# Optimization experiments

Measured on AMD Instinct MI355X. Metric: run time of the kernel, lower is better.

The kernel has to match this reference:

```python
import jax, jax.numpy as jnp
import numpy as np

H = 512      # hidden_size
NH = 8       # head_size (num heads)
DH = H // NH # att_size per head
FFN = 2048
B, S = 8, 1024
NEG = -1e9
EPS = 1e-5


def _layernorm(x, g, b):
    mu = jnp.mean(x, axis=-1, keepdims=True)
    var = jnp.var(x, axis=-1, keepdims=True)
    return (x - mu) * jax.lax.rsqrt(var + EPS) * g + b


def setup_inputs() -> dict:
    key = jax.random.key(0)
    ks = jax.random.split(key, 16)
    s = 0.02
    return {
        "x": jax.random.normal(ks[0], (B, S, H), jnp.float32),
        "attn_bias": jax.random.normal(ks[1], (B, S, S), jnp.float32),
        "graph_mask": jax.random.randint(ks[2], (B, S, S), 0, 2, jnp.int32),
        "ln1_g": jnp.ones((H,), jnp.float32),
        "ln1_b": jnp.zeros((H,), jnp.float32),
        "Wq": jax.random.normal(ks[3], (H, H), jnp.float32) * s,
        "bq": jnp.zeros((H,), jnp.float32),
        "Wk": jax.random.normal(ks[4], (H, H), jnp.float32) * s,
        "bk": jnp.zeros((H,), jnp.float32),
        "Wv": jax.random.normal(ks[5], (H, H), jnp.float32) * s,
        "bv": jnp.zeros((H,), jnp.float32),
        "Wo": jax.random.normal(ks[6], (H, H), jnp.float32) * s,
        "bo": jnp.zeros((H,), jnp.float32),
        "ln2_g": jnp.ones((H,), jnp.float32),
        "ln2_b": jnp.zeros((H,), jnp.float32),
        "W1": jax.random.normal(ks[7], (H, FFN), jnp.float32) * s,
        "b1": jnp.zeros((FFN,), jnp.float32),
        "W2": jax.random.normal(ks[8], (FFN, H), jnp.float32) * s,
        "b2": jnp.zeros((H,), jnp.float32),
    }


def reference(x, attn_bias, graph_mask, ln1_g, ln1_b, Wq, bq, Wk, bk, Wv, bv,
              Wo, bo, ln2_g, ln2_b, W1, b1, W2, b2):
    b, s, h = x.shape
    # --- self-attention block (eval mode: dropouts are identity) ---
    y = _layernorm(x, ln1_g, ln1_b)
    q = (y @ Wq + bq).reshape(b, s, NH, DH).transpose(0, 2, 1, 3)  # [B,h,S,d]
    k = (y @ Wk + bk).reshape(b, s, NH, DH).transpose(0, 2, 1, 3)
    v = (y @ Wv + bv).reshape(b, s, NH, DH).transpose(0, 2, 1, 3)
    scale = DH ** -0.5
    scores = jnp.einsum('bhqd,bhkd->bhqk', q * scale, k)  # [B,h,S,S]
    mask = (graph_mask == 0)[:, None, :, :]               # [B,1,S,S] broadcast over heads
    bias = jnp.where(mask, NEG, attn_bias[:, None, :, :])
    scores = scores + bias
    scores = jnp.where(mask, NEG, scores)
    p = jax.nn.softmax(scores, axis=-1)
    o = jnp.einsum('bhqk,bhkd->bhqd', p, v)
    o = o.transpose(0, 2, 1, 3).reshape(b, s, h) @ Wo + bo
    x = x + o
    # --- FFN block ---
    y = _layernorm(x, ln2_g, ln2_b)
    y = jax.nn.gelu(y @ W1 + b1, approximate=False) @ W2 + b2
    return x + y
```

## Files before the change

### kernel.cpp

```cpp
#include <hip/hip_runtime.h>
#include <hip/hip_bf16.h>
#include <type_traits>

static constexpr int kS   = 1024;
static constexpr int kH   = 512;
static constexpr int kFFN = 2048;

using bf16 = __hip_bfloat16;
using short8  = __attribute__((ext_vector_type(8))) short;
using float4v = __attribute__((ext_vector_type(4))) float;
#define MFMA16 __builtin_amdgcn_mfma_f32_16x16x32_bf16

__device__ __forceinline__ unsigned short f2bfu(float f){
  unsigned int u = __float_as_uint(f);
  return (unsigned short)((u + 0x7fffu + ((u >> 16) & 1u)) >> 16);
}
__device__ __forceinline__ float bfu2f(unsigned short u){
  return __uint_as_float(((unsigned int)u) << 16);
}
__device__ __forceinline__ unsigned int pack2(float a, float b){
  return (unsigned int)f2bfu(a) | ((unsigned int)f2bfu(b) << 16);
}
__device__ __forceinline__ void async16(const void* g, void* l){
  __builtin_amdgcn_global_load_lds(
    (const __attribute__((address_space(1))) unsigned int*)g,
    (__attribute__((address_space(3))) unsigned int*)l, 16, 0, 0);
}
__device__ __forceinline__ int swz(int col, int row){
  return (col & ~63) | (((((col>>3)&7) ^ (row&7)))<<3) | (col&7);
}

__device__ __forceinline__ void ln_row(const float* __restrict__ x,
    const float* __restrict__ g, const float* __restrict__ bb,
    bf16* __restrict__ y, long row, int lane){
  const float* xr = x + row * kH + lane*8;
  float4 a = *(const float4*)xr, c = *(const float4*)(xr+4);
  float v[8] = {a.x,a.y,a.z,a.w,c.x,c.y,c.z,c.w};
  float s=0.f, s2=0.f;
#pragma unroll
  for(int i=0;i<8;i++){ s += v[i]; s2 += v[i]*v[i]; }
#pragma unroll
  for(int o=32; o>=1; o>>=1){ s += __shfl_xor(s,o,64); s2 += __shfl_xor(s2,o,64); }
  float mu  = s * (1.f/kH);
  float rs  = rsqrtf(s2*(1.f/kH) - mu*mu + 1e-5f);
  float gv[8], bv[8];
  {
    float4 t0=*(const float4*)(g+lane*8),  t1=*(const float4*)(g+lane*8+4);
    float4 t2=*(const float4*)(bb+lane*8), t3=*(const float4*)(bb+lane*8+4);
    gv[0]=t0.x;gv[1]=t0.y;gv[2]=t0.z;gv[3]=t0.w;gv[4]=t1.x;gv[5]=t1.y;gv[6]=t1.z;gv[7]=t1.w;
    bv[0]=t2.x;bv[1]=t2.y;bv[2]=t2.z;bv[3]=t2.w;bv[4]=t3.x;bv[5]=t3.y;bv[6]=t3.z;bv[7]=t3.w;
  }
  unsigned int ow[4];
#pragma unroll
  for(int i=0;i<4;i++){
    float a0 = (v[2*i]  -mu)*rs*gv[2*i]   + bv[2*i];
    float a1 = (v[2*i+1]-mu)*rs*gv[2*i+1] + bv[2*i+1];
    ow[i] = pack2(a0, a1);
  }
  *reinterpret_cast<uint4*>(y + row*kH + swz(lane*8, (int)row)) = make_uint4(ow[0],ow[1],ow[2],ow[3]);
}

__global__ __launch_bounds__(256) void ln_kernel(const float* __restrict__ x,
    const float* __restrict__ g, const float* __restrict__ bb, bf16* __restrict__ y){
  ln_row(x, g, bb, y, (long)blockIdx.x*4 + (threadIdx.x>>6), threadIdx.x&63);
}

__device__ __forceinline__ void prep_tile(const float* __restrict__ W,
    bf16* __restrict__ WT, int K, int N, int kb, int nb){
  __shared__ unsigned short Ts[64*68];
  int tid=threadIdx.x;
  {
    int k=tid>>2, nc=(tid&3)*16;
    const float* p = W + (size_t)(kb+k)*N + nb+nc;
#pragma unroll
    for(int i=0;i<16;i+=4){
      float4 f = *(const float4*)(p+i);
      Ts[k*68+nc+i  ]=f2bfu(f.x); Ts[k*68+nc+i+1]=f2bfu(f.y);
      Ts[k*68+nc+i+2]=f2bfu(f.z); Ts[k*68+nc+i+3]=f2bfu(f.w);
    }
  }
  __syncthreads();
  {
    int n=tid>>2, kc=(tid&3)*16;
    unsigned short tmp[16];
#pragma unroll
    for(int i=0;i<16;i++) tmp[i] = Ts[(kc+i)*68 + n];
    int row = nb+n, kg0 = kc>>3;
    bf16* op = WT + (size_t)row*K + kb;
    *(uint4*)(op + (((kg0  ^(row&7)))<<3)) = *(uint4*)&tmp[0];
    *(uint4*)(op + ((((kg0+1)^(row&7)))<<3)) = *(uint4*)&tmp[8];
  }
}

__global__ __launch_bounds__(256) void ln1_prep_qkv(
    const float* __restrict__ x, const float* __restrict__ g, const float* __restrict__ bb,
    bf16* __restrict__ y, const float* __restrict__ Wq, const float* __restrict__ Wk,
    const float* __restrict__ Wv, bf16* __restrict__ WT){
  int id = blockIdx.x;
  if(id < 2048){
    ln_row(x, g, bb, y, (long)id*4 + (threadIdx.x>>6), threadIdx.x&63);
  } else {
    int pid = id - 2048, sel = pid>>6, lid = pid&63;
    const float* W = sel==0 ? Wq : (sel==1 ? Wk : Wv);
    prep_tile(W, WT + (size_t)sel*262144, kH, kH, (lid>>3)*64, (lid&7)*64);
  }
}

__global__ __launch_bounds__(256) void prep_rest(
    const float* __restrict__ Wo, const float* __restrict__ W1, const float* __restrict__ W2,
    bf16* __restrict__ WoT, bf16* __restrict__ W1T, bf16* __restrict__ W2T){
  int id = blockIdx.x;
  const float* W; bf16* WT; int K, N, kb, nb;
  if(id < 64)       { W=Wo; WT=WoT; K=kH;   N=kH;   kb=(id>>3)*64;        nb=(id&7)*64; }
  else if(id < 320) { int l=id-64;  W=W1; WT=W1T; K=kH;   N=kFFN; kb=(l>>5)*64; nb=(l&31)*64; }
  else              { int l=id-320; W=W2; WT=W2T; K=kFFN; N=kH;   kb=(l>>3)*64; nb=(l&7)*64; }
  prep_tile(W, WT, K, N, kb, nb);
}

__global__ __launch_bounds__(256) void bias_eff_kernel(
    const int* __restrict__ mask, const float* __restrict__ bias, bf16* __restrict__ be){
  size_t i8 = ((size_t)blockIdx.x*256 + threadIdx.x)*8;
  int4   m0 = *(const int4*)(mask+i8),   m1 = *(const int4*)(mask+i8+4);
  float4 b0 = *(const float4*)(bias+i8), b1 = *(const float4*)(bias+i8+4);
  const unsigned short NEG = f2bfu(-1e9f);
  unsigned short o[8];
  o[0]=m0.x?f2bfu(b0.x):NEG; o[1]=m0.y?f2bfu(b0.y):NEG;
  o[2]=m0.z?f2bfu(b0.z):NEG; o[3]=m0.w?f2bfu(b0.w):NEG;
  o[4]=m1.x?f2bfu(b1.x):NEG; o[5]=m1.y?f2bfu(b1.y):NEG;
  o[6]=m1.z?f2bfu(b1.z):NEG; o[7]=m1.w?f2bfu(b1.w):NEG;
  *(uint4*)((unsigned short*)be + i8) = *(uint4*)o;
}

template<int BM, int BN, typename OutT, bool SCALE, bool GELU, bool RES, bool CSW>
__global__ __launch_bounds__((BM/64)*(BN/64)*64, 3) void mfma_gemm(
    const bf16* __restrict__ A, const bf16* __restrict__ BT,
    const float* __restrict__ bias, const float* __restrict__ res,
    OutT* __restrict__ C, int M, int N, int K)
{
  constexpr int W  = (BM/64)*(BN/64);
  constexpr int NW = BN/64;
  constexpr int AC = (BM/8)/W, BC = (BN/8)/W;
  __shared__ __align__(16) unsigned short As[BM*64];
  __shared__ __align__(16) unsigned short Bs[BN*64];
  int tid=threadIdx.x, lane=tid&63, quad=lane>>4, l16=lane&15;
  int w=__builtin_amdgcn_readfirstlane(tid>>6);
  int wr = w / NW, wc = w % NW;
  int m0=blockIdx.y*BM, n0=blockIdx.x*BN;
  int lr=lane>>3, lc=lane&7;
  float4v acc[4][4] = {};
  for(int k0=0;k0<K;k0+=64){
    __syncthreads();
#pragma unroll
    for(int i=0;i<AC;i++){
      int r = (w*AC+i)*8;
      async16(A + (size_t)(m0+r+lr)*K + k0 + lc*8, &As[r*64]);
    }
#pragma unroll
    for(int i=0;i<BC;i++){
      int r = (w*BC+i)*8;
      async16(BT + (size_t)(n0+r+lr)*K + k0 + lc*8, &Bs[r*64]);
    }
    __syncthreads();
#pragma unroll
    for(int hf=0;hf<2;hf++){
      short8 af[4], bfv[4];
#pragma unroll
      for(int mi=0;mi<4;mi++){
        int row=wr*64+mi*16+l16;
        af[mi]=*(const short8*)&As[row*64 + (((hf*4+quad)^(row&7))<<3)];
      }
#pragma unroll
      for(int ni=0;ni<4;ni++){
        int n=wc*64+ni*16+l16;
        bfv[ni]=*(const short8*)&Bs[n*64 + (((hf*4+quad)^(n&7))<<3)];
      }
#pragma unroll
      for(int ni=0;ni<4;ni++)
#pragma unroll
        for(int mi=0;mi<4;mi++)
          acc[mi][ni]=MFMA16(af[mi],bfv[ni],acc[mi][ni],0,0,0);
    }
  }
#pragma unroll
  for(int ni=0;ni<4;ni++){
    int col=n0+wc*64+ni*16+l16;
    float bc=bias[col];
#pragma unroll
    for(int mi=0;mi<4;mi++){
#pragma unroll
      for(int r=0;r<4;r++){
        int row=m0+wr*64+mi*16+quad*4+r;
        float v=acc[mi][ni][r]+bc;
        if constexpr(SCALE) v*=0.125f;
        if constexpr(GELU)  v=0.5f*v*(1.f+erff(v*0.70710678118f));
        size_t idx=(size_t)row*N+col;
        if constexpr(RES) v+=res[idx];
        if constexpr(std::is_same<OutT,float>::value) C[idx]=v;
        else {
          size_t ix = CSW ? ((size_t)row*N + swz(col,row)) : idx;
          reinterpret_cast<unsigned short*>(C)[ix]=f2bfu(v);
        }
      }
    }
  }
}

__global__ __launch_bounds__(256, 4) void quad_gemm(
    const bf16* __restrict__ A, const bf16* __restrict__ BT,
    const float* __restrict__ bias, const float* __restrict__ res,
    float* __restrict__ C, int M, int N, int K)
{
  __shared__ __align__(16) unsigned short As[64*64];
  __shared__ __align__(16) unsigned short Bs[64*64];
  int tid=threadIdx.x, lane=tid&63, quad=lane>>4, l16=lane&15;
  int w=__builtin_amdgcn_readfirstlane(tid>>6);
  int wr=w>>1, wc=w&1;
  int m0=blockIdx.y*64, n0=blockIdx.x*64;
  int lr=lane>>3, lc=lane&7;
  float4v acc[2][2]={};
  for(int k0=0;k0<K;k0+=64){
    __syncthreads();
#pragma unroll
    for(int i=0;i<2;i++){
      int r=(w*2+i)*8;
      async16(A  + (size_t)(m0+r+lr)*K + k0 + lc*8, &As[r*64]);
      async16(BT + (size_t)(n0+r+lr)*K + k0 + lc*8, &Bs[r*64]);
    }
    __syncthreads();
#pragma unroll
    for(int hf=0;hf<2;hf++){
      short8 af[2], bfv[2];
#pragma unroll
      for(int mi=0;mi<2;mi++){
        int row=wr*32+mi*16+l16;
        af[mi]=*(const short8*)&As[row*64 + (((hf*4+quad)^(row&7))<<3)];
      }
#pragma unroll
      for(int ni=0;ni<2;ni++){
        int n=wc*32+ni*16+l16;
        bfv[ni]=*(const short8*)&Bs[n*64 + (((hf*4+quad)^(n&7))<<3)];
      }
#pragma unroll
      for(int ni=0;ni<2;ni++)
#pragma unroll
        for(int mi=0;mi<2;mi++)
          acc[mi][ni]=MFMA16(af[mi],bfv[ni],acc[mi][ni],0,0,0);
    }
  }
#pragma unroll
  for(int ni=0;ni<2;ni++){
    int col=n0+wc*32+ni*16+l16;
    float bc=bias[col];
#pragma unroll
    for(int mi=0;mi<2;mi++){
#pragma unroll
      for(int r=0;r<4;r++){
        int row=m0+wr*32+mi*16+quad*4+r;
        float v=acc[mi][ni][r]+bc;
        size_t idx=(size_t)row*N+col;
        v+=res[idx];
        C[idx]=v;
      }
    }
  }
}

__global__ __launch_bounds__(256, 3) void mfma_gemm_qkv(
    const bf16* __restrict__ A, const bf16* __restrict__ BT,
    const float* __restrict__ bq, const float* __restrict__ bk, const float* __restrict__ bv,
    bf16* __restrict__ qo, bf16* __restrict__ ko, bf16* __restrict__ vT, int M, int N, int K)
{
  __shared__ __align__(16) unsigned short As[128*64];
  __shared__ __align__(16) unsigned short Bs[128*64];
  int tid=threadIdx.x, lane=tid&63, quad=lane>>4, l16=lane&15;
  int w=__builtin_amdgcn_readfirstlane(tid>>6);
  int wr = w >> 1, wc = w & 1;
  int m0=blockIdx.y*128, n0=blockIdx.x*128;
  int lr=lane>>3, lc=lane&7;
  float4v acc[4][4] = {};
  for(int k0=0;k0<K;k0+=64){
    __syncthreads();
#pragma unroll
    for(int i=0;i<4;i++){
      int r = (w*4+i)*8;
      async16(A + (size_t)(m0+r+lr)*K + k0 + lc*8, &As[r*64]);
    }
#pragma unroll
    for(int i=0;i<4;i++){
      int r = (w*4+i)*8;
      async16(BT + (size_t)(n0+r+lr)*K + k0 + lc*8, &Bs[r*64]);
    }
    __syncthreads();
#pragma unroll
    for(int hf=0;hf<2;hf++){
      short8 af[4], bfv[4];
#pragma unroll
      for(int mi=0;mi<4;mi++){
        int row=wr*64+mi*16+l16;
        af[mi]=*(const short8*)&As[row*64 + (((hf*4+quad)^(row&7))<<3)];
      }
#pragma unroll
      for(int ni=0;ni<4;ni++){
        int n=wc*64+ni*16+l16;
        bfv[ni]=*(const short8*)&Bs[n*64 + (((hf*4+quad)^(n&7))<<3)];
      }
#pragma unroll
      for(int ni=0;ni<4;ni++)
#pragma unroll
        for(int mi=0;mi<4;mi++)
          acc[mi][ni]=MFMA16(af[mi],bfv[ni],acc[mi][ni],0,0,0);
    }
  }
  int sec = __builtin_amdgcn_readfirstlane(n0 >> 9);
  const float* bp = sec==0 ? bq : (sec==1 ? bk : bv);
  if(sec == 2){
#pragma unroll
    for(int ni=0;ni<4;ni++){
      int cl=(n0+wc*64+ni*16+l16)&511;
      float bc=bp[cl];
#pragma unroll
      for(int mi=0;mi<4;mi++){
        int row0=m0+wr*64+mi*16+quad*4;
        unsigned int p0=pack2(acc[mi][ni][0]+bc, acc[mi][ni][1]+bc);
        unsigned int p1=pack2(acc[mi][ni][2]+bc, acc[mi][ni][3]+bc);
        *reinterpret_cast<uint2*>(reinterpret_cast<unsigned short*>(vT)
            + (size_t)cl*8192 + row0) = make_uint2(p0,p1);
      }
    }
  } else {
    unsigned short* dst = (unsigned short*)(sec==0 ? qo : ko);
    float scl = (sec==0) ? 0.125f : 1.0f;
#pragma unroll
    for(int ni=0;ni<4;ni++){
      int col=n0+wc*64+ni*16+l16, cl=col&511;
      float bc=bp[cl];
#pragma unroll
      for(int mi=0;mi<4;mi++){
#pragma unroll
        for(int r=0;r<4;r++){
          int row=m0+wr*64+mi*16+quad*4+r;
          dst[(size_t)row*512+cl]=f2bfu((acc[mi][ni][r]+bc)*scl);
        }
      }
    }
  }
}

__global__ __launch_bounds__(256,3) void attn_mfma(
    const bf16* __restrict__ q, const bf16* __restrict__ k,
    const bf16* __restrict__ vT, const bf16* __restrict__ be,
    bf16* __restrict__ o)
{
  __shared__ __align__(16) unsigned short Ks[2][64*64];
  __shared__ __align__(16) unsigned short Vt[2][64*64];
  __shared__ __align__(16) unsigned short Ps[4*16*72];
  int tid=threadIdx.x, lane=tid&63, quad=lane>>4, l16=lane&15;
  int w=__builtin_amdgcn_readfirstlane(tid>>6);
  int lin = blockIdx.y*16 + blockIdx.x;
  int nid = (lin&7)*128 + (lin>>3);
  int q0=(nid&15)*64, bh=nid>>4, b=bh>>3, h=bh&7;
  int lr=lane>>3, lc=lane&7;
  const bf16* qp = q + (size_t)(b*kS + q0 + w*16 + l16)*kH + h*64;
  short8 aq0 = *(const short8*)(qp + quad*8);
  short8 aq1 = *(const short8*)(qp + 32 + quad*8);
  float lpart[4]={0.f,0.f,0.f,0.f};
  float4v oacc[4]={};
  int pb = w*16*72;
  int rql = w*16 + quad*4;
  const unsigned short* beRow[4];
#pragma unroll
  for(int r=0;r<4;r++)
    beRow[r] = reinterpret_cast<const unsigned short*>(be) + (size_t)(b*kS+q0+rql+r)*kS + l16;

  auto stage = [&](int kt, int bufi){
    int kb = kt*64;
#pragma unroll
    for(int i=0;i<2;i++){
      int rr = w*16 + i*8;
      async16(k  + (size_t)(b*kS+kb+rr+lr)*kH + h*64 + ((lc^lr)<<3), &Ks[bufi][rr*64]);
      async16(vT + (size_t)(h*64+rr+lr)*8192 + b*kS + kb + ((lc^lr)<<3), &Vt[bufi][rr*64]);
    }
  };
  stage(0,0);
  __syncthreads();
  for(int kt=0;kt<16;kt++){
    int cur=kt&1, kb=kt*64;
    float bev[4][4];
#pragma unroll
    for(int t=0;t<4;t++)
#pragma unroll
      for(int r=0;r<4;r++)
        bev[t][r] = bfu2f(beRow[r][kb + t*16]);
    if(kt<15) stage(kt+1, cur^1);
    float4v sa[4];
#pragma unroll
    for(int t=0;t<4;t++){
      int krow=t*16+l16, kx=krow&7;
      short8 b0 = *(const short8*)&Ks[cur][krow*64 + ((quad^kx)<<3)];
      short8 b1 = *(const short8*)&Ks[cur][krow*64 + (((4+quad)^kx)<<3)];
      float4v ci;
#pragma unroll
      for(int r=0;r<4;r++) ci[r] = bev[t][r];
      ci = MFMA16(aq0,b0,ci,0,0,0);
      sa[t]=MFMA16(aq1,b1,ci,0,0,0);
    }
#pragma unroll
    for(int t=0;t<4;t++){
      int kg = t*2 + (l16>>3), j = l16&7;
#pragma unroll
      for(int r=0;r<4;r++){
        float p = __expf(sa[t][r] - 24.f);
        lpart[r] += p;
        int row = quad*4+r;
        Ps[pb + row*72 + ((kg^(row&7))<<3) + j] = f2bfu(p);
      }
    }
    short8 ap0 = *(const short8*)&Ps[pb + l16*72 + ((quad^(l16&7))<<3)];
    short8 ap1 = *(const short8*)&Ps[pb + l16*72 + (((4+quad)^(l16&7))<<3)];
#pragma unroll
    for(int dt=0;dt<4;dt++){
      int vrow=dt*16+l16, vx=vrow&7;
      short8 bv0=*(const short8*)&Vt[cur][vrow*64+((quad^vx)<<3)];
      short8 bv1=*(const short8*)&Vt[cur][vrow*64+(((4+quad)^vx)<<3)];
      oacc[dt]=MFMA16(ap0,bv0,oacc[dt],0,0,0);
      oacc[dt]=MFMA16(ap1,bv1,oacc[dt],0,0,0);
    }
    __syncthreads();
  }
  float inv[4];
#pragma unroll
  for(int r=0;r<4;r++){
    float l = lpart[r];
    l += __shfl_xor(l,1,64); l += __shfl_xor(l,2,64);
    l += __shfl_xor(l,4,64); l += __shfl_xor(l,8,64);
    inv[r] = 1.f/l;
  }
#pragma unroll
  for(int dt=0;dt<4;dt++)
#pragma unroll
    for(int r=0;r<4;r++){
      int row = b*kS + q0 + rql + r;
      int col = h*64 + dt*16 + l16;
      reinterpret_cast<unsigned short*>(o)[(size_t)row*kH + swz(col,row)] =
        f2bfu(oacc[dt][r]*inv[r]);
    }
}

extern "C" void kernel_launch(void* const* d_in, const int* in_sizes, int n_in,
                              void* d_out, int out_size, void* d_ws, size_t ws_size,
                              hipStream_t stream){
  (void)in_sizes; (void)n_in; (void)out_size; (void)ws_size;
  const float* x         = (const float*)d_in[0];
  const float* attn_bias = (const float*)d_in[1];
  const int*   graph_mask= (const int*)  d_in[2];
  const float* ln1_g = (const float*)d_in[3];
  const float* ln1_b = (const float*)d_in[4];
  const float* Wq = (const float*)d_in[5];
  const float* bq = (const float*)d_in[6];
  const float* Wk = (const float*)d_in[7];
  const float* bk = (const float*)d_in[8];
  const float* Wv = (const float*)d_in[9];
  const float* bv = (const float*)d_in[10];
  const float* Wo = (const float*)d_in[11];
  const float* bo = (const float*)d_in[12];
  const float* ln2_g = (const float*)d_in[13];
  const float* ln2_b = (const float*)d_in[14];
  const float* W1 = (const float*)d_in[15];
  const float* b1 = (const float*)d_in[16];
  const float* W2 = (const float*)d_in[17];
  const float* b2 = (const float*)d_in[18];

  char* wsb = (char*)d_ws;
  const size_t SZ = (size_t)8192 * kH * sizeof(bf16);
  bf16* s0 = (bf16*)(wsb);
  bf16* s1 = (bf16*)(wsb + SZ);
  bf16* s2 = (bf16*)(wsb + 2*SZ);
  bf16* s3 = (bf16*)(wsb + 3*SZ);
  float* outf = (float*)d_out;
  bf16*  WqkvT = (bf16*)d_out;
  bf16*  beP   = (bf16*)d_out;
  bf16* WoT = s3;
  bf16* W1T = s3 + 262144;
  bf16* W2T = s3 + 262144 + 1048576;

  dim3 blk(256);
  ln1_prep_qkv<<<dim3(2240), blk, 0, stream>>>(x, ln1_g, ln1_b, s0, Wq, Wk, Wv, WqkvT);
  mfma_gemm_qkv<<<dim3(12,64), blk, 0, stream>>>(s0, WqkvT, bq, bk, bv, s1, s2, s3, 8192, 3*kH, kH);
  bias_eff_kernel<<<dim3(4096), blk, 0, stream>>>(graph_mask, attn_bias, beP);
  attn_mfma<<<dim3(16,64), blk, 0, stream>>>(s1, s2, s3, beP, s0);
  prep_rest<<<dim3(576), blk, 0, stream>>>(Wo, W1, W2, WoT, W1T, W2T);
  quad_gemm<<<dim3(8,128), blk, 0, stream>>>(s0, WoT, bo, x, outf, 8192, kH, kH);
  ln_kernel<<<dim3(2048), blk, 0, stream>>>(outf, ln2_g, ln2_b, s0);
  for(int c=0;c<2;c++){
    size_t ro = (size_t)c * 4096 * kH;
    mfma_gemm<128,128,bf16,false,true ,false,true ><<<dim3(16,32), blk, 0, stream>>>(s0 + ro, W1T, b1, nullptr, s1, 4096, kFFN, kH);
    quad_gemm<<<dim3(8,64), blk, 0, stream>>>(s1, W2T, b2, outf + ro, outf + ro, 4096, kH, kFFN);
  }
}
```

Baseline: 330.4 us.

## Process 32 query rows per wave in attention to reuse K/V tiles

```diff
diff --git a/kernel.cpp b/kernel.cpp
--- a/kernel.cpp
+++ b/kernel.cpp
@@ -346,31 +346,37 @@
   }
 }
 
-__global__ __launch_bounds__(256,3) void attn_mfma(
+__global__ __launch_bounds__(256,2) void attn_mfma(
     const bf16* __restrict__ q, const bf16* __restrict__ k,
     const bf16* __restrict__ vT, const bf16* __restrict__ be,
     bf16* __restrict__ o)
 {
   __shared__ __align__(16) unsigned short Ks[2][64*64];
   __shared__ __align__(16) unsigned short Vt[2][64*64];
-  __shared__ __align__(16) unsigned short Ps[4*16*72];
+  __shared__ __align__(16) unsigned short Ps[4*32*72];
   int tid=threadIdx.x, lane=tid&63, quad=lane>>4, l16=lane&15;
   int w=__builtin_amdgcn_readfirstlane(tid>>6);
-  int lin = blockIdx.y*16 + blockIdx.x;
-  int nid = (lin&7)*128 + (lin>>3);
-  int q0=(nid&15)*64, bh=nid>>4, b=bh>>3, h=bh&7;
+  int lin = blockIdx.x;
+  int nid = (lin&7)*64 + (lin>>3);
+  int q0=(nid&7)*128, bh=nid>>3, b=bh>>3, h=bh&7;
   int lr=lane>>3, lc=lane&7;
-  const bf16* qp = q + (size_t)(b*kS + q0 + w*16 + l16)*kH + h*64;
-  short8 aq0 = *(const short8*)(qp + quad*8);
-  short8 aq1 = *(const short8*)(qp + 32 + quad*8);
-  float lpart[4]={0.f,0.f,0.f,0.f};
-  float4v oacc[4]={};
-  int pb = w*16*72;
-  int rql = w*16 + quad*4;
-  const unsigned short* beRow[4];
-#pragma unroll
-  for(int r=0;r<4;r++)
-    beRow[r] = reinterpret_cast<const unsigned short*>(be) + (size_t)(b*kS+q0+rql+r)*kS + l16;
+  short8 aq[2][2];
+#pragma unroll
+  for(int g=0;g<2;g++){
+    const bf16* qp = q + (size_t)(b*kS + q0 + w*32 + g*16 + l16)*kH + h*64;
+    aq[g][0] = *(const short8*)(qp + quad*8);
+    aq[g][1] = *(const short8*)(qp + 32 + quad*8);
+  }
+  float lpart[2][4]={};
+  float4v oacc[2][4]={};
+  int pb = w*32*72;
+  const unsigned short* beRow[2][4];
+#pragma unroll
+  for(int g=0;g<2;g++)
+#pragma unroll
+    for(int r=0;r<4;r++)
+      beRow[g][r] = reinterpret_cast<const unsigned short*>(be)
+                  + (size_t)(b*kS+q0+w*32+g*16+quad*4+r)*kS + l16;
 
   auto stage = [&](int kt, int bufi){
     int kb = kt*64;
@@ -381,69 +387,97 @@
       async16(vT + (size_t)(h*64+rr+lr)*8192 + b*kS + kb + ((lc^lr)<<3), &Vt[bufi][rr*64]);
     }
   };
+  float bevc[2][4][4];
   stage(0,0);
+#pragma unroll
+  for(int g=0;g<2;g++)
+#pragma unroll
+    for(int r=0;r<4;r++)
+#pragma unroll
+      for(int t=0;t<4;t++)
+        bevc[g][r][t] = bfu2f(beRow[g][r][t*16]);
   __syncthreads();
   for(int kt=0;kt<16;kt++){
-    int cur=kt&1, kb=kt*64;
-    float bev[4][4];
-#pragma unroll
-    for(int t=0;t<4;t++)
-#pragma unroll
-      for(int r=0;r<4;r++)
-        bev[t][r] = bfu2f(beRow[r][kb + t*16]);
+    int cur=kt&1;
     if(kt<15) stage(kt+1, cur^1);
-    float4v sa[4];
+    float4v sa[2][4];
 #pragma unroll
     for(int t=0;t<4;t++){
       int krow=t*16+l16, kx=krow&7;
       short8 b0 = *(const short8*)&Ks[cur][krow*64 + ((quad^kx)<<3)];
       short8 b1 = *(const short8*)&Ks[cur][krow*64 + (((4+quad)^kx)<<3)];
-      float4v ci;
-#pragma unroll
-      for(int r=0;r<4;r++) ci[r] = bev[t][r];
-      ci = MFMA16(aq0,b0,ci,0,0,0);
-      sa[t]=MFMA16(aq1,b1,ci,0,0,0);
-    }
+#pragma unroll
+      for(int g=0;g<2;g++){
+        float4v ci;
+#pragma unroll
+        for(int r=0;r<4;r++) ci[r] = bevc[g][r][t];
+        ci = MFMA16(aq[g][0],b0,ci,0,0,0);
+        sa[g][t]=MFMA16(aq[g][1],b1,ci,0,0,0);
+      }
+    }
+    if(kt<15){
+      int kb2=(kt+1)*64;
+#pragma unroll
+      for(int g=0;g<2;g++)
+#pragma unroll
+        for(int r=0;r<4;r++)
+#pragma unroll
+          for(int t=0;t<4;t++)
+            bevc[g][r][t] = bfu2f(beRow[g][r][kb2 + t*16]);
+    }
+#pragma unroll
+    for(int g=0;g<2;g++)
 #pragma unroll
     for(int t=0;t<4;t++){
       int kg = t*2 + (l16>>3), j = l16&7;
 #pragma unroll
       for(int r=0;r<4;r++){
-        float p = __expf(sa[t][r] - 24.f);
-        lpart[r] += p;
-        int row = quad*4+r;
+        float p = __expf(sa[g][t][r] - 24.f);
+        lpart[g][r] += p;
+        int row = g*16 + quad*4+r;
         Ps[pb + row*72 + ((kg^(row&7))<<3) + j] = f2bfu(p);
       }
     }
-    short8 ap0 = *(const short8*)&Ps[pb + l16*72 + ((quad^(l16&7))<<3)];
-    short8 ap1 = *(const short8*)&Ps[pb + l16*72 + (((4+quad)^(l16&7))<<3)];
+    short8 ap[2][2];
+#pragma unroll
+    for(int g=0;g<2;g++){
+      int prow = g*16 + l16;
+      ap[g][0] = *(const short8*)&Ps[pb + prow*72 + ((quad^(prow&7))<<3)];
+      ap[g][1] = *(const short8*)&Ps[pb + prow*72 + (((4+quad)^(prow&7))<<3)];
+    }
 #pragma unroll
     for(int dt=0;dt<4;dt++){
       int vrow=dt*16+l16, vx=vrow&7;
       short8 bv0=*(const short8*)&Vt[cur][vrow*64+((quad^vx)<<3)];
       short8 bv1=*(const short8*)&Vt[cur][vrow*64+(((4+quad)^vx)<<3)];
-      oacc[dt]=MFMA16(ap0,bv0,oacc[dt],0,0,0);
-      oacc[dt]=MFMA16(ap1,bv1,oacc[dt],0,0,0);
-    }
-    __syncthreads();
-  }
-  float inv[4];
-#pragma unroll
-  for(int r=0;r<4;r++){
-    float l = lpart[r];
-    l += __shfl_xor(l,1,64); l += __shfl_xor(l,2,64);
-    l += __shfl_xor(l,4,64); l += __shfl_xor(l,8,64);
-    inv[r] = 1.f/l;
-  }
-#pragma unroll
-  for(int dt=0;dt<4;dt++)
+#pragma unroll
+      for(int g=0;g<2;g++){
+        oacc[g][dt]=MFMA16(ap[g][0],bv0,oacc[g][dt],0,0,0);
+        oacc[g][dt]=MFMA16(ap[g][1],bv1,oacc[g][dt],0,0,0);
+      }
+    }
+    __syncthreads();
+  }
+#pragma unroll
+  for(int g=0;g<2;g++){
+    float inv[4];
 #pragma unroll
     for(int r=0;r<4;r++){
-      int row = b*kS + q0 + rql + r;
-      int col = h*64 + dt*16 + l16;
-      reinterpret_cast<unsigned short*>(o)[(size_t)row*kH + swz(col,row)] =
-        f2bfu(oacc[dt][r]*inv[r]);
-    }
+      float l = lpart[g][r];
+      l += __shfl_xor(l,1,64); l += __shfl_xor(l,2,64);
+      l += __shfl_xor(l,4,64); l += __shfl_xor(l,8,64);
+      inv[r] = 1.f/l;
+    }
+#pragma unroll
+    for(int dt=0;dt<4;dt++)
+#pragma unroll
+      for(int r=0;r<4;r++){
+        int row = b*kS + q0 + w*32 + g*16 + quad*4 + r;
+        int col = h*64 + dt*16 + l16;
+        reinterpret_cast<unsigned short*>(o)[(size_t)row*kH + swz(col,row)] =
+          f2bfu(oacc[g][dt][r]*inv[r]);
+      }
+  }
 }
 
 extern "C" void kernel_launch(void* const* d_in, const int* in_sizes, int n_in,
@@ -487,7 +521,7 @@
   ln1_prep_qkv<<<dim3(2240), blk, 0, stream>>>(x, ln1_g, ln1_b, s0, Wq, Wk, Wv, WqkvT);
   mfma_gemm_qkv<<<dim3(12,64), blk, 0, stream>>>(s0, WqkvT, bq, bk, bv, s1, s2, s3, 8192, 3*kH, kH);
   bias_eff_kernel<<<dim3(4096), blk, 0, stream>>>(graph_mask, attn_bias, beP);
-  attn_mfma<<<dim3(16,64), blk, 0, stream>>>(s1, s2, s3, beP, s0);
+  attn_mfma<<<dim3(512), blk, 0, stream>>>(s1, s2, s3, beP, s0);
   prep_rest<<<dim3(576), blk, 0, stream>>>(Wo, W1, W2, WoT, W1T, W2T);
   quad_gemm<<<dim3(8,128), blk, 0, stream>>>(s0, WoT, bo, x, outf, 8192, kH, kH);
   ln_kernel<<<dim3(2048), blk, 0, stream>>>(outf, ln2_g, ln2_b, s0);
```

Measured after the change: 326.6 us. No clear change (-1.2%).
